# Performance work log

Measured on AMD Instinct MI355X. Metric: run time of the kernel, lower is better.

## Reference

```python
import jax, jax.numpy as jnp
import numpy as np

N_NODES = 100000
N_EDGES = 1000000
IN_F, HID_F, OUT_F = 64, 64, 32


def setup_inputs() -> dict:
    key = jax.random.key(0)
    ks = jax.random.split(key, 9)
    x = jax.random.normal(ks[0], (N_NODES, IN_F), dtype=jnp.float32)
    edge_index = jax.random.randint(ks[1], (2, N_EDGES), 0, N_NODES, dtype=jnp.int64)
    edge_attr = jax.random.uniform(ks[2], (N_EDGES,), dtype=jnp.float32)
    def glorot(k, shape):
        fan_in = shape[1]
        return jax.random.normal(k, shape, dtype=jnp.float32) / jnp.sqrt(jnp.float32(fan_in))
    # PyG GraphConv: lin_rel (with bias) applied to aggregated neighbors,
    # lin_root (no bias) applied to self features.
    W_rel1 = glorot(ks[3], (HID_F, IN_F))
    b_rel1 = jnp.zeros((HID_F,), dtype=jnp.float32)
    W_root1 = glorot(ks[4], (HID_F, IN_F))
    W_rel2 = glorot(ks[5], (OUT_F, HID_F))
    b_rel2 = jnp.zeros((OUT_F,), dtype=jnp.float32)
    W_root2 = glorot(ks[6], (OUT_F, HID_F))
    return {"x": x, "edge_index": edge_index, "edge_attr": edge_attr,
            "W_rel1": W_rel1, "b_rel1": b_rel1, "W_root1": W_root1,
            "W_rel2": W_rel2, "b_rel2": b_rel2, "W_root2": W_root2}


def graph_conv(h, edge_index, edge_attr, W_rel, b_rel, W_root, num_nodes):
    src, dst = edge_index[0], edge_index[1]
    # message: edge_weight * x_src  -> [E, F]
    msg = h[src] * edge_attr[:, None]
    agg = jax.ops.segment_sum(msg, dst, num_segments=num_nodes)
    cnt = jax.ops.segment_sum(jnp.ones_like(edge_attr), dst, num_segments=num_nodes)
    agg = agg / jnp.maximum(cnt, 1.0)[:, None]  # mean aggregation
    return agg @ W_rel.T + b_rel + h @ W_root.T


def reference(x, edge_index, edge_attr, W_rel1, b_rel1, W_root1, W_rel2, b_rel2, W_root2):
    n = x.shape[0]
    h = graph_conv(x, edge_index, edge_attr, W_rel1, b_rel1, W_root1, n)
    h = jax.nn.sigmoid(h)
    return graph_conv(h, edge_index, edge_attr, W_rel2, b_rel2, W_root2, n)
```

## Files before the change

kernel.cpp:

```cpp
#include <hip/hip_runtime.h>
#include <hip/hip_bf16.h>


#define NF 64
#define CSHIFT 7
#define CMASK 127
#define CMAX 1024

typedef __attribute__((ext_vector_type(8))) short bf16x8;
typedef __attribute__((ext_vector_type(4))) float f32x4;

__device__ __forceinline__ unsigned short f2bf(float f) {
    __hip_bfloat16 h = __float2bfloat16(f);
    return *reinterpret_cast<unsigned short*>(&h);
}
__device__ __forceinline__ float bf2f(unsigned short u) {
    return __uint_as_float((unsigned int)u << 16);
}

__global__ __launch_bounds__(256) void prep(
    const unsigned* __restrict__ raw, int* __restrict__ flag, int E,
    const float* __restrict__ Wrel1, const float* __restrict__ Wroot1,
    const float* __restrict__ Wrel2, const float* __restrict__ Wroot2,
    unsigned short* __restrict__ Wp1rel, unsigned short* __restrict__ Wp1root,
    unsigned short* __restrict__ Wp2,
    const float* __restrict__ x, unsigned short* __restrict__ xb, long long n4)
{
    if (blockIdx.x == 0) {
        __shared__ unsigned red[256];
        unsigned v = 0;
        int lim = (E < 4096) ? E : 4096;
        for (int i = threadIdx.x; i < lim; i += 256) v |= raw[2 * i + 1];
        red[threadIdx.x] = v;
        __syncthreads();
        for (int s = 128; s > 0; s >>= 1) {
            if (threadIdx.x < s) red[threadIdx.x] |= red[threadIdx.x + s];
            __syncthreads();
        }
        if (threadIdx.x == 0) *flag = (red[0] == 0) ? 1 : 0;
    } else if (blockIdx.x == 1) {
        for (int i = threadIdx.x; i < 4096; i += 256) {
            int b = i & 7, l = (i >> 3) & 63, nt = (i >> 9) & 3, kc = i >> 11;
            int j = nt * 16 + (l & 15);
            int k = kc * 32 + ((l >> 4) << 3) + b;
            Wp1rel[i]  = f2bf(Wrel1[j * 64 + k]);
            Wp1root[i] = f2bf(Wroot1[j * 64 + k]);
            Wp2[i]     = f2bf((j < 32) ? Wrel2[j * 64 + k]
                                       : Wroot2[(j - 32) * 64 + k]);
        }
    } else {
        long long i = (long long)(blockIdx.x - 2) * 256 + threadIdx.x;
        long long stride = (long long)(gridDim.x - 2) * 256;
        for (; i < n4; i += stride) {
            float4 v = *(const float4*)(x + i * 4);
            ushort4 o;
            o.x = f2bf(v.x); o.y = f2bf(v.y); o.z = f2bf(v.z); o.w = f2bf(v.w);
            *(ushort4*)(xb + i * 4) = o;
        }
    }
}

__global__ __launch_bounds__(1024) void p1_hist(const void* __restrict__ raw,
                                                const int* __restrict__ flag,
                                                int* __restrict__ hb,
                                                int E, int C, int B1) {
    __shared__ int cnt[CMAX];
    int t = threadIdx.x;
    for (int i = t; i < C; i += 1024) cnt[i] = 0;
    __syncthreads();
    int fl = *flag;
    int ebase = blockIdx.x * 4096;
#pragma unroll
    for (int j = 0; j < 4; ++j) {
        int e = ebase + j * 1024 + t;
        if (e < E) {
            int d = fl ? (int)((const long long*)raw)[E + e] : ((const int*)raw)[E + e];
            atomicAdd(&cnt[d >> CSHIFT], 1);
        }
    }
    __syncthreads();
    for (int i = t; i < C; i += 1024) hb[i * B1 + blockIdx.x] = cnt[i];
}

__global__ __launch_bounds__(1024) void scan_k1(const int* __restrict__ in,
                                                int* __restrict__ out,
                                                int* __restrict__ bsums, int M) {
    __shared__ int tmp[1024];
    int tid = threadIdx.x;
    int i = blockIdx.x * 1024 + tid;
    int v = (i < M) ? in[i] : 0;
    tmp[tid] = v;
    __syncthreads();
    for (int off = 1; off < 1024; off <<= 1) {
        int t = (tid >= off) ? tmp[tid - off] : 0;
        __syncthreads();
        tmp[tid] += t;
        __syncthreads();
    }
    if (i < M) out[i] = tmp[tid] - v;
    if (tid == 1023) bsums[blockIdx.x] = tmp[tid];
}

__global__ __launch_bounds__(1024) void scan_k2(int* __restrict__ bsums, int nb) {
    __shared__ int tmp[1024];
    int tid = threadIdx.x;
    int v = (tid < nb) ? bsums[tid] : 0;
    tmp[tid] = v;
    __syncthreads();
    for (int off = 1; off < 1024; off <<= 1) {
        int t = (tid >= off) ? tmp[tid - off] : 0;
        __syncthreads();
        tmp[tid] += t;
        __syncthreads();
    }
    if (tid < nb) bsums[tid] = tmp[tid] - v;
}

__global__ __launch_bounds__(1024) void scan_k3(int* __restrict__ out,
                                                const int* __restrict__ bsums, int M) {
    int i = blockIdx.x * 1024 + threadIdx.x;
    if (i >= M) return;
    out[i] += bsums[blockIdx.x];
}

__global__ __launch_bounds__(1024) void p3_scatter(const void* __restrict__ raw,
                                                   const int* __restrict__ flag,
                                                   const float* __restrict__ ea,
                                                   const int* __restrict__ off,
                                                   long long* __restrict__ part,
                                                   int E, int C, int B1) {
    __shared__ int lcur[CMAX];
    int t = threadIdx.x;
    for (int i = t; i < C; i += 1024) lcur[i] = off[i * B1 + blockIdx.x];
    __syncthreads();
    int fl = *flag;
    int ebase = blockIdx.x * 4096;
#pragma unroll
    for (int j = 0; j < 4; ++j) {
        int e = ebase + j * 1024 + t;
        if (e < E) {
            int s, d;
            if (fl) { const long long* p = (const long long*)raw; s = (int)p[e]; d = (int)p[E + e]; }
            else    { const int* p = (const int*)raw; s = p[e]; d = p[E + e]; }
            float w = ea[e];
            int slot = atomicAdd(&lcur[d >> CSHIFT], 1);
            long long pk = (unsigned int)(s | ((d & CMASK) << 20))
                         | ((long long)__float_as_int(w) << 32);
            part[slot] = pk;
        }
    }
}

__global__ __launch_bounds__(256) void p4_build(const int* __restrict__ off,
                                                const long long* __restrict__ part,
                                                int2* __restrict__ csr,
                                                int* __restrict__ deg,
                                                int* __restrict__ base,
                                                int E, int N, int C, int B1) {
    __shared__ int ldeg[128], tmp[128], lcur[128];
    int c = blockIdx.x, t = threadIdx.x;
    int bstart = off[c * B1];
    int bend = (c + 1 < C) ? off[(c + 1) * B1] : E;
    if (t < 128) ldeg[t] = 0;
    __syncthreads();
    for (int i = bstart + t; i < bend; i += 256) {
        int lo = (int)part[i];
        atomicAdd(&ldeg[(lo >> 20) & CMASK], 1);
    }
    __syncthreads();
    if (t < 128) tmp[t] = ldeg[t];
    __syncthreads();
    for (int o = 1; o < 128; o <<= 1) {
        int v = (t < 128 && t >= o) ? tmp[t - o] : 0;
        __syncthreads();
        if (t < 128) tmp[t] += v;
        __syncthreads();
    }
    if (t < 128) {
        int ex = tmp[t] - ldeg[t];
        lcur[t] = ex;
        int n = (c << CSHIFT) + t;
        if (n < N) { deg[n] = ldeg[t]; base[n] = bstart + ex; }
    }
    __syncthreads();
    for (int i = bstart + t; i < bend; i += 256) {
        long long pk = part[i];
        int lo = (int)pk;
        int r = atomicAdd(&lcur[(lo >> 20) & CMASK], 1);
        csr[bstart + r] = make_int2(lo & 0xFFFFF, (int)(pk >> 32));
    }
}

__global__ __launch_bounds__(256) void gather1(
    const unsigned short* __restrict__ xb, const int2* __restrict__ csr,
    const int* __restrict__ base, const int* __restrict__ deg,
    unsigned short* __restrict__ aggb, int N)
{
    int lane = threadIdx.x & 63;
    int wid = blockIdx.x * 4 + (threadIdx.x >> 6);
    int stride = gridDim.x * 4;
    for (int n = wid; n < N; n += stride) {
        int b = __builtin_amdgcn_readfirstlane(base[n]);
        int dg = __builtin_amdgcn_readfirstlane(deg[n]);
        float acc0 = 0.f, acc1 = 0.f, acc2 = 0.f, acc3 = 0.f;
        int i = b, e = b + dg;
        for (; i + 8 <= e; i += 8) {
            int2 r0 = csr[i], r1 = csr[i + 1], r2 = csr[i + 2], r3 = csr[i + 3];
            int2 r4 = csr[i + 4], r5 = csr[i + 5], r6 = csr[i + 6], r7 = csr[i + 7];
            float v0 = bf2f(xb[(size_t)r0.x * 64 + lane]);
            float v1 = bf2f(xb[(size_t)r1.x * 64 + lane]);
            float v2 = bf2f(xb[(size_t)r2.x * 64 + lane]);
            float v3 = bf2f(xb[(size_t)r3.x * 64 + lane]);
            float v4 = bf2f(xb[(size_t)r4.x * 64 + lane]);
            float v5 = bf2f(xb[(size_t)r5.x * 64 + lane]);
            float v6 = bf2f(xb[(size_t)r6.x * 64 + lane]);
            float v7 = bf2f(xb[(size_t)r7.x * 64 + lane]);
            acc0 = fmaf(__int_as_float(r0.y), v0, acc0);
            acc1 = fmaf(__int_as_float(r1.y), v1, acc1);
            acc2 = fmaf(__int_as_float(r2.y), v2, acc2);
            acc3 = fmaf(__int_as_float(r3.y), v3, acc3);
            acc0 = fmaf(__int_as_float(r4.y), v4, acc0);
            acc1 = fmaf(__int_as_float(r5.y), v5, acc1);
            acc2 = fmaf(__int_as_float(r6.y), v6, acc2);
            acc3 = fmaf(__int_as_float(r7.y), v7, acc3);
        }
        for (; i + 4 <= e; i += 4) {
            int2 r0 = csr[i], r1 = csr[i + 1], r2 = csr[i + 2], r3 = csr[i + 3];
            acc0 = fmaf(__int_as_float(r0.y), bf2f(xb[(size_t)r0.x * 64 + lane]), acc0);
            acc1 = fmaf(__int_as_float(r1.y), bf2f(xb[(size_t)r1.x * 64 + lane]), acc1);
            acc2 = fmaf(__int_as_float(r2.y), bf2f(xb[(size_t)r2.x * 64 + lane]), acc2);
            acc3 = fmaf(__int_as_float(r3.y), bf2f(xb[(size_t)r3.x * 64 + lane]), acc3);
        }
        for (; i < e; ++i) {
            int2 r = csr[i];
            acc0 = fmaf(__int_as_float(r.y), bf2f(xb[(size_t)r.x * 64 + lane]), acc0);
        }
        float inv = 1.0f / fmaxf((float)dg, 1.0f);
        aggb[(size_t)n * 64 + lane] = f2bf(((acc0 + acc1) + (acc2 + acc3)) * inv);
    }
}

__global__ __launch_bounds__(256) void node_mfma(
    const unsigned short* __restrict__ aggb, const unsigned short* __restrict__ xb,
    const unsigned short* __restrict__ Wp1rel, const unsigned short* __restrict__ Wp1root,
    const unsigned short* __restrict__ Wp2,
    const float* __restrict__ brel1, const float* __restrict__ brel2,
    unsigned short* __restrict__ hrb, float* __restrict__ hro, int N)
{
    __shared__ unsigned short hx[64 * 72];
    int t = threadIdx.x;
    int lane = t & 63;
    int w = t >> 6;
    int col = lane & 15;
    int kg = lane >> 4;
    int n0 = blockIdx.x * 64;
    int rowA = n0 + w * 16 + col;
    size_t rowAc = (size_t)((rowA < N) ? rowA : (N - 1)) * 64;

    const bf16x8* B1r = (const bf16x8*)Wp1rel;
    const bf16x8* B1o = (const bf16x8*)Wp1root;
    const bf16x8* B2  = (const bf16x8*)Wp2;

    f32x4 acc0, acc1, acc2, acc3;
    {
        float b0 = brel1[col], b1 = brel1[16 + col];
        float b2 = brel1[32 + col], b3 = brel1[48 + col];
        acc0 = (f32x4){b0, b0, b0, b0};
        acc1 = (f32x4){b1, b1, b1, b1};
        acc2 = (f32x4){b2, b2, b2, b2};
        acc3 = (f32x4){b3, b3, b3, b3};
    }

#define MFMA __builtin_amdgcn_mfma_f32_16x16x32_bf16
#pragma unroll
    for (int kc = 0; kc < 2; ++kc) {
        bf16x8 a = *(const bf16x8*)(aggb + rowAc + kc * 32 + kg * 8);
        acc0 = MFMA(a, B1r[(kc * 4 + 0) * 64 + lane], acc0, 0, 0, 0);
        acc1 = MFMA(a, B1r[(kc * 4 + 1) * 64 + lane], acc1, 0, 0, 0);
        acc2 = MFMA(a, B1r[(kc * 4 + 2) * 64 + lane], acc2, 0, 0, 0);
        acc3 = MFMA(a, B1r[(kc * 4 + 3) * 64 + lane], acc3, 0, 0, 0);
    }
#pragma unroll
    for (int kc = 0; kc < 2; ++kc) {
        bf16x8 a = *(const bf16x8*)(xb + rowAc + kc * 32 + kg * 8);
        acc0 = MFMA(a, B1o[(kc * 4 + 0) * 64 + lane], acc0, 0, 0, 0);
        acc1 = MFMA(a, B1o[(kc * 4 + 1) * 64 + lane], acc1, 0, 0, 0);
        acc2 = MFMA(a, B1o[(kc * 4 + 2) * 64 + lane], acc2, 0, 0, 0);
        acc3 = MFMA(a, B1o[(kc * 4 + 3) * 64 + lane], acc3, 0, 0, 0);
    }

#define SIG4(A) \
    A[0] = 1.f / (1.f + __expf(-A[0])); A[1] = 1.f / (1.f + __expf(-A[1])); \
    A[2] = 1.f / (1.f + __expf(-A[2])); A[3] = 1.f / (1.f + __expf(-A[3]));
    SIG4(acc0) SIG4(acc1) SIG4(acc2) SIG4(acc3)
#undef SIG4

    {
        int rbase = (w * 16 + 4 * kg) * 72;
#define STORE_H(V)                                                       \
        hx[rbase + (V) * 72 + col]      = f2bf(acc0[V]);                 \
        hx[rbase + (V) * 72 + 16 + col] = f2bf(acc1[V]);                 \
        hx[rbase + (V) * 72 + 32 + col] = f2bf(acc2[V]);                 \
        hx[rbase + (V) * 72 + 48 + col] = f2bf(acc3[V]);
        STORE_H(0) STORE_H(1) STORE_H(2) STORE_H(3)
#undef STORE_H
    }
    __syncthreads();

    acc0 = (f32x4){0.f, 0.f, 0.f, 0.f};
    acc1 = (f32x4){0.f, 0.f, 0.f, 0.f};
    {
        float b2a = brel2[col], b2b = brel2[16 + col];
        acc2 = (f32x4){b2a, b2a, b2a, b2a};
        acc3 = (f32x4){b2b, b2b, b2b, b2b};
    }
#pragma unroll
    for (int kc = 0; kc < 2; ++kc) {
        bf16x8 a = *(const bf16x8*)(&hx[(w * 16 + col) * 72 + kc * 32 + kg * 8]);
        acc0 = MFMA(a, B2[(kc * 4 + 0) * 64 + lane], acc0, 0, 0, 0);
        acc1 = MFMA(a, B2[(kc * 4 + 1) * 64 + lane], acc1, 0, 0, 0);
        acc2 = MFMA(a, B2[(kc * 4 + 2) * 64 + lane], acc2, 0, 0, 0);
        acc3 = MFMA(a, B2[(kc * 4 + 3) * 64 + lane], acc3, 0, 0, 0);
    }
#undef MFMA

    {
        int nbase = n0 + w * 16 + 4 * kg;
#define STORE_OUT(V)                                                        \
        if (nbase + (V) < N) {                                              \
            size_t r32 = (size_t)(nbase + (V)) * 32;                        \
            hrb[r32 + col]      = f2bf(acc0[V]);                            \
            hrb[r32 + 16 + col] = f2bf(acc1[V]);                            \
            hro[r32 + col]      = acc2[V];                                  \
            hro[r32 + 16 + col] = acc3[V];                                  \
        }
        STORE_OUT(0) STORE_OUT(1) STORE_OUT(2) STORE_OUT(3)
#undef STORE_OUT
    }
}

__global__ __launch_bounds__(256) void gather2(
    const unsigned short* __restrict__ hrb, const float* __restrict__ hro,
    const int2* __restrict__ csr, const int* __restrict__ base,
    const int* __restrict__ deg, float* __restrict__ out, int N)
{
    int lane = threadIdx.x & 63;
    int j = lane & 31, half = lane >> 5;
    int wid = blockIdx.x * 4 + (threadIdx.x >> 6);
    int stride = gridDim.x * 4;
    for (int n = wid; n < N; n += stride) {
        int b = __builtin_amdgcn_readfirstlane(base[n]);
        int dg = __builtin_amdgcn_readfirstlane(deg[n]);
        float a0 = 0.f, a1 = 0.f, a2 = 0.f, a3 = 0.f;
        int i = b + half, e = b + dg;
        for (; i + 8 <= e + half; i += 8) {
            int2 r0 = csr[i], r1 = csr[i + 2], r2 = csr[i + 4], r3 = csr[i + 6];
            a0 = fmaf(__int_as_float(r0.y), bf2f(hrb[(size_t)r0.x * 32 + j]), a0);
            a1 = fmaf(__int_as_float(r1.y), bf2f(hrb[(size_t)r1.x * 32 + j]), a1);
            a2 = fmaf(__int_as_float(r2.y), bf2f(hrb[(size_t)r2.x * 32 + j]), a2);
            a3 = fmaf(__int_as_float(r3.y), bf2f(hrb[(size_t)r3.x * 32 + j]), a3);
        }
        for (; i < e; i += 2) {
            int2 r = csr[i];
            a0 = fmaf(__int_as_float(r.y), bf2f(hrb[(size_t)r.x * 32 + j]), a0);
        }
        float acc = (a0 + a1) + (a2 + a3);
        acc += __shfl_xor(acc, 32);
        if (half == 0) {
            float inv = 1.0f / fmaxf((float)dg, 1.0f);
            out[(size_t)n * 32 + j] = acc * inv + hro[(size_t)n * 32 + j];
        }
    }
}

extern "C" void kernel_launch(void* const* d_in, const int* in_sizes, int n_in,
                              void* d_out, int out_size, void* d_ws, size_t ws_size,
                              hipStream_t stream) {
    const float* x      = (const float*)d_in[0];
    const void*  ei_raw = d_in[1];
    const float* ea     = (const float*)d_in[2];
    const float* Wrel1  = (const float*)d_in[3];
    const float* brel1  = (const float*)d_in[4];
    const float* Wroot1 = (const float*)d_in[5];
    const float* Wrel2  = (const float*)d_in[6];
    const float* brel2  = (const float*)d_in[7];
    const float* Wroot2 = (const float*)d_in[8];
    float* out = (float*)d_out;

    const int N = in_sizes[0] / NF;
    const int E = in_sizes[2];
    const int C  = (N + CMASK) >> CSHIFT;
    const int B1 = (E + 4095) / 4096;
    const int M  = C * B1;
    const int nbM = (M + 1023) / 1024;

    long long* part = (long long*)d_ws;
    int2*  csr     = (int2*)(part + E);
    int*   off     = (int*)(csr + E);
    int*   bsums   = off + M;
    int*   flag    = bsums + 1024;
    int*   deg     = flag + 4;
    int*   base    = deg + N;
    float* hro     = (float*)(base + N);
    unsigned short* xb     = (unsigned short*)(hro + (size_t)N * 32);
    unsigned short* aggb   = xb + (size_t)N * 64;
    unsigned short* hrb    = aggb + (size_t)N * 64;
    unsigned short* Wp1rel = hrb + (size_t)N * 32;
    unsigned short* Wp1root= Wp1rel + 4096;
    unsigned short* Wp2    = Wp1root + 4096;

    prep<<<2048, 256, 0, stream>>>((const unsigned*)ei_raw, flag, E,
                                   Wrel1, Wroot1, Wrel2, Wroot2,
                                   Wp1rel, Wp1root, Wp2, x, xb, (long long)N * 16);
    p1_hist<<<B1, 1024, 0, stream>>>(ei_raw, flag, (int*)csr, E, C, B1);
    scan_k1<<<nbM, 1024, 0, stream>>>((int*)csr, off, bsums, M);
    scan_k2<<<1, 1024, 0, stream>>>(bsums, nbM);
    scan_k3<<<nbM, 1024, 0, stream>>>(off, bsums, M);
    p3_scatter<<<B1, 1024, 0, stream>>>(ei_raw, flag, ea, off, part, E, C, B1);
    p4_build<<<C, 256, 0, stream>>>(off, part, csr, deg, base, E, N, C, B1);

    gather1<<<2048, 256, 0, stream>>>(xb, csr, base, deg, aggb, N);
    node_mfma<<<(N + 63) / 64, 256, 0, stream>>>(aggb, xb, Wp1rel, Wp1root, Wp2,
                                                 brel1, brel2, hrb, hro, N);
    gather2<<<2048, 256, 0, stream>>>(hrb, hro, csr, base, deg, out, N);
}
```

Before: 137.7 us.

## Restructure layer-2 gather as per-chunk block with LDS atomic accumulation

```diff
diff --git a/kernel.cpp b/kernel.cpp
--- a/kernel.cpp
+++ b/kernel.cpp
@@ -187,7 +187,7 @@
         long long pk = part[i];
         int lo = (int)pk;
         int r = atomicAdd(&lcur[(lo >> 20) & CMASK], 1);
-        csr[bstart + r] = make_int2(lo & 0xFFFFF, (int)(pk >> 32));
+        csr[bstart + r] = make_int2(lo & 0x07FFFFFF, (int)(pk >> 32));
     }
 }
 
@@ -207,14 +207,14 @@
         for (; i + 8 <= e; i += 8) {
             int2 r0 = csr[i], r1 = csr[i + 1], r2 = csr[i + 2], r3 = csr[i + 3];
             int2 r4 = csr[i + 4], r5 = csr[i + 5], r6 = csr[i + 6], r7 = csr[i + 7];
-            float v0 = bf2f(xb[(size_t)r0.x * 64 + lane]);
-            float v1 = bf2f(xb[(size_t)r1.x * 64 + lane]);
-            float v2 = bf2f(xb[(size_t)r2.x * 64 + lane]);
-            float v3 = bf2f(xb[(size_t)r3.x * 64 + lane]);
-            float v4 = bf2f(xb[(size_t)r4.x * 64 + lane]);
-            float v5 = bf2f(xb[(size_t)r5.x * 64 + lane]);
-            float v6 = bf2f(xb[(size_t)r6.x * 64 + lane]);
-            float v7 = bf2f(xb[(size_t)r7.x * 64 + lane]);
+            float v0 = bf2f(xb[(size_t)(r0.x & 0xFFFFF) * 64 + lane]);
+            float v1 = bf2f(xb[(size_t)(r1.x & 0xFFFFF) * 64 + lane]);
+            float v2 = bf2f(xb[(size_t)(r2.x & 0xFFFFF) * 64 + lane]);
+            float v3 = bf2f(xb[(size_t)(r3.x & 0xFFFFF) * 64 + lane]);
+            float v4 = bf2f(xb[(size_t)(r4.x & 0xFFFFF) * 64 + lane]);
+            float v5 = bf2f(xb[(size_t)(r5.x & 0xFFFFF) * 64 + lane]);
+            float v6 = bf2f(xb[(size_t)(r6.x & 0xFFFFF) * 64 + lane]);
+            float v7 = bf2f(xb[(size_t)(r7.x & 0xFFFFF) * 64 + lane]);
             acc0 = fmaf(__int_as_float(r0.y), v0, acc0);
             acc1 = fmaf(__int_as_float(r1.y), v1, acc1);
             acc2 = fmaf(__int_as_float(r2.y), v2, acc2);
@@ -226,14 +226,14 @@
         }
         for (; i + 4 <= e; i += 4) {
             int2 r0 = csr[i], r1 = csr[i + 1], r2 = csr[i + 2], r3 = csr[i + 3];
-            acc0 = fmaf(__int_as_float(r0.y), bf2f(xb[(size_t)r0.x * 64 + lane]), acc0);
-            acc1 = fmaf(__int_as_float(r1.y), bf2f(xb[(size_t)r1.x * 64 + lane]), acc1);
-            acc2 = fmaf(__int_as_float(r2.y), bf2f(xb[(size_t)r2.x * 64 + lane]), acc2);
-            acc3 = fmaf(__int_as_float(r3.y), bf2f(xb[(size_t)r3.x * 64 + lane]), acc3);
+            acc0 = fmaf(__int_as_float(r0.y), bf2f(xb[(size_t)(r0.x & 0xFFFFF) * 64 + lane]), acc0);
+            acc1 = fmaf(__int_as_float(r1.y), bf2f(xb[(size_t)(r1.x & 0xFFFFF) * 64 + lane]), acc1);
+            acc2 = fmaf(__int_as_float(r2.y), bf2f(xb[(size_t)(r2.x & 0xFFFFF) * 64 + lane]), acc2);
+            acc3 = fmaf(__int_as_float(r3.y), bf2f(xb[(size_t)(r3.x & 0xFFFFF) * 64 + lane]), acc3);
         }
         for (; i < e; ++i) {
             int2 r = csr[i];
-            acc0 = fmaf(__int_as_float(r.y), bf2f(xb[(size_t)r.x * 64 + lane]), acc0);
+            acc0 = fmaf(__int_as_float(r.y), bf2f(xb[(size_t)(r.x & 0xFFFFF) * 64 + lane]), acc0);
         }
         float inv = 1.0f / fmaxf((float)dg, 1.0f);
         aggb[(size_t)n * 64 + lane] = f2bf(((acc0 + acc1) + (acc2 + acc3)) * inv);
@@ -341,34 +341,46 @@
 
 __global__ __launch_bounds__(256) void gather2(
     const unsigned short* __restrict__ hrb, const float* __restrict__ hro,
-    const int2* __restrict__ csr, const int* __restrict__ base,
-    const int* __restrict__ deg, float* __restrict__ out, int N)
+    const int2* __restrict__ csr, const int* __restrict__ off,
+    const int* __restrict__ deg, float* __restrict__ out,
+    int E, int N, int C, int B1)
 {
-    int lane = threadIdx.x & 63;
-    int j = lane & 31, half = lane >> 5;
-    int wid = blockIdx.x * 4 + (threadIdx.x >> 6);
-    int stride = gridDim.x * 4;
-    for (int n = wid; n < N; n += stride) {
-        int b = __builtin_amdgcn_readfirstlane(base[n]);
-        int dg = __builtin_amdgcn_readfirstlane(deg[n]);
-        float a0 = 0.f, a1 = 0.f, a2 = 0.f, a3 = 0.f;
-        int i = b + half, e = b + dg;
-        for (; i + 8 <= e + half; i += 8) {
-            int2 r0 = csr[i], r1 = csr[i + 2], r2 = csr[i + 4], r3 = csr[i + 6];
-            a0 = fmaf(__int_as_float(r0.y), bf2f(hrb[(size_t)r0.x * 32 + j]), a0);
-            a1 = fmaf(__int_as_float(r1.y), bf2f(hrb[(size_t)r1.x * 32 + j]), a1);
-            a2 = fmaf(__int_as_float(r2.y), bf2f(hrb[(size_t)r2.x * 32 + j]), a2);
-            a3 = fmaf(__int_as_float(r3.y), bf2f(hrb[(size_t)r3.x * 32 + j]), a3);
-        }
-        for (; i < e; i += 2) {
-            int2 r = csr[i];
-            a0 = fmaf(__int_as_float(r.y), bf2f(hrb[(size_t)r.x * 32 + j]), a0);
-        }
-        float acc = (a0 + a1) + (a2 + a3);
-        acc += __shfl_xor(acc, 32);
-        if (half == 0) {
-            float inv = 1.0f / fmaxf((float)dg, 1.0f);
-            out[(size_t)n * 32 + j] = acc * inv + hro[(size_t)n * 32 + j];
+    __shared__ float acc[128 * 32];
+    int t = threadIdx.x;
+    int c = blockIdx.x;
+    int bstart = off[c * B1];
+    int bend = (c + 1 < C) ? off[(c + 1) * B1] : E;
+    for (int i = t; i < 4096; i += 256) acc[i] = 0.f;
+    __syncthreads();
+
+    int j = t & 31;
+    int eslot = t >> 5;
+    int i = bstart + eslot;
+    for (; i + 32 <= bend; i += 32) {
+        int2 r0 = csr[i],      r1 = csr[i + 8];
+        int2 r2 = csr[i + 16], r3 = csr[i + 24];
+        float v0 = bf2f(hrb[(size_t)(r0.x & 0xFFFFF) * 32 + j]);
+        float v1 = bf2f(hrb[(size_t)(r1.x & 0xFFFFF) * 32 + j]);
+        float v2 = bf2f(hrb[(size_t)(r2.x & 0xFFFFF) * 32 + j]);
+        float v3 = bf2f(hrb[(size_t)(r3.x & 0xFFFFF) * 32 + j]);
+        atomicAdd(&acc[(((r0.x >> 20) & 127) << 5) + j], __int_as_float(r0.y) * v0);
+        atomicAdd(&acc[(((r1.x >> 20) & 127) << 5) + j], __int_as_float(r1.y) * v1);
+        atomicAdd(&acc[(((r2.x >> 20) & 127) << 5) + j], __int_as_float(r2.y) * v2);
+        atomicAdd(&acc[(((r3.x >> 20) & 127) << 5) + j], __int_as_float(r3.y) * v3);
+    }
+    for (; i < bend; i += 8) {
+        int2 r = csr[i];
+        float v = bf2f(hrb[(size_t)(r.x & 0xFFFFF) * 32 + j]);
+        atomicAdd(&acc[(((r.x >> 20) & 127) << 5) + j], __int_as_float(r.y) * v);
+    }
+    __syncthreads();
+
+    for (int o = t; o < 4096; o += 256) {
+        int dl = o >> 5, jj = o & 31;
+        int n = (c << CSHIFT) + dl;
+        if (n < N) {
+            float inv = 1.0f / fmaxf((float)deg[n], 1.0f);
+            out[(size_t)n * 32 + jj] = acc[o] * inv + hro[(size_t)n * 32 + jj];
         }
     }
 }
@@ -422,5 +434,5 @@
     gather1<<<2048, 256, 0, stream>>>(xb, csr, base, deg, aggb, N);
     node_mfma<<<(N + 63) / 64, 256, 0, stream>>>(aggb, xb, Wp1rel, Wp1root, Wp2,
                                                  brel1, brel2, hrb, hro, N);
-    gather2<<<2048, 256, 0, stream>>>(hrb, hro, csr, base, deg, out, N);
-}
+    gather2<<<C, 256, 0, stream>>>(hrb, hro, csr, off, deg, out, E, N, C, B1);
+}
```

Measured after the change: 316.1 us. +129.5%, slower.

## Process four nodes per wavefront in gather2 with packed bf16 pair loads

Applied to the files above, without the earlier changes.

```diff
diff --git a/kernel.cpp b/kernel.cpp
--- a/kernel.cpp
+++ b/kernel.cpp
@@ -345,30 +345,51 @@
     const int* __restrict__ deg, float* __restrict__ out, int N)
 {
     int lane = threadIdx.x & 63;
-    int j = lane & 31, half = lane >> 5;
+    int q = lane >> 4;
+    int fl = lane & 15;
     int wid = blockIdx.x * 4 + (threadIdx.x >> 6);
     int stride = gridDim.x * 4;
-    for (int n = wid; n < N; n += stride) {
-        int b = __builtin_amdgcn_readfirstlane(base[n]);
-        int dg = __builtin_amdgcn_readfirstlane(deg[n]);
+    for (int g = wid * 4; g < N; g += stride * 4) {
+        int n = g + q;
+        bool valid = n < N;
+        int nc = valid ? n : (N - 1);
+        int b = base[nc];
+        int dg = deg[nc];
         float a0 = 0.f, a1 = 0.f, a2 = 0.f, a3 = 0.f;
-        int i = b + half, e = b + dg;
-        for (; i + 8 <= e + half; i += 8) {
-            int2 r0 = csr[i], r1 = csr[i + 2], r2 = csr[i + 4], r3 = csr[i + 6];
-            a0 = fmaf(__int_as_float(r0.y), bf2f(hrb[(size_t)r0.x * 32 + j]), a0);
-            a1 = fmaf(__int_as_float(r1.y), bf2f(hrb[(size_t)r1.x * 32 + j]), a1);
-            a2 = fmaf(__int_as_float(r2.y), bf2f(hrb[(size_t)r2.x * 32 + j]), a2);
-            a3 = fmaf(__int_as_float(r3.y), bf2f(hrb[(size_t)r3.x * 32 + j]), a3);
-        }
-        for (; i < e; i += 2) {
+        float b0 = 0.f, b1 = 0.f, b2 = 0.f, b3 = 0.f;
+        int i = b, e = b + dg;
+        for (; i + 4 <= e; i += 4) {
+            int2 r0 = csr[i], r1 = csr[i + 1], r2 = csr[i + 2], r3 = csr[i + 3];
+            unsigned u0 = *(const unsigned*)(hrb + (size_t)r0.x * 32 + fl * 2);
+            unsigned u1 = *(const unsigned*)(hrb + (size_t)r1.x * 32 + fl * 2);
+            unsigned u2 = *(const unsigned*)(hrb + (size_t)r2.x * 32 + fl * 2);
+            unsigned u3 = *(const unsigned*)(hrb + (size_t)r3.x * 32 + fl * 2);
+            float w0 = __int_as_float(r0.y), w1 = __int_as_float(r1.y);
+            float w2 = __int_as_float(r2.y), w3 = __int_as_float(r3.y);
+            a0 = fmaf(w0, __uint_as_float(u0 << 16), a0);
+            b0 = fmaf(w0, __uint_as_float(u0 & 0xffff0000u), b0);
+            a1 = fmaf(w1, __uint_as_float(u1 << 16), a1);
+            b1 = fmaf(w1, __uint_as_float(u1 & 0xffff0000u), b1);
+            a2 = fmaf(w2, __uint_as_float(u2 << 16), a2);
+            b2 = fmaf(w2, __uint_as_float(u2 & 0xffff0000u), b2);
+            a3 = fmaf(w3, __uint_as_float(u3 << 16), a3);
+            b3 = fmaf(w3, __uint_as_float(u3 & 0xffff0000u), b3);
+        }
+        for (; i < e; ++i) {
             int2 r = csr[i];
-            a0 = fmaf(__int_as_float(r.y), bf2f(hrb[(size_t)r.x * 32 + j]), a0);
-        }
-        float acc = (a0 + a1) + (a2 + a3);
-        acc += __shfl_xor(acc, 32);
-        if (half == 0) {
+            unsigned u = *(const unsigned*)(hrb + (size_t)r.x * 32 + fl * 2);
+            float w = __int_as_float(r.y);
+            a0 = fmaf(w, __uint_as_float(u << 16), a0);
+            b0 = fmaf(w, __uint_as_float(u & 0xffff0000u), b0);
+        }
+        if (valid) {
             float inv = 1.0f / fmaxf((float)dg, 1.0f);
-            out[(size_t)n * 32 + j] = acc * inv + hro[(size_t)n * 32 + j];
+            float s0 = ((a0 + a1) + (a2 + a3)) * inv;
+            float s1 = ((b0 + b1) + (b2 + b3)) * inv;
+            const float* hsrc = hro + (size_t)n * 32 + fl * 2;
+            float2 hv = *(const float2*)hsrc;
+            *(float2*)(out + (size_t)n * 32 + fl * 2) =
+                make_float2(s0 + hv.x, s1 + hv.y);
         }
     }
 }
```

New measurement: 123.6 us. 1.11x faster.
